# Kernel optimization log

Measured on AMD Instinct MI355X. Metric: run time of the kernel, lower is better.

Reference implementation:

```python
import jax, jax.numpy as jnp
import numpy as np

NUM_HEADS = 8
SIZES = [(80, 80), (40, 40), (20, 20), (10, 10), (5, 5)]


def _ln(x, g, b):
    m = x.mean(-1, keepdims=True)
    var = ((x - m) ** 2).mean(-1, keepdims=True)
    return (x - m) / jnp.sqrt(var + 1e-5) * g + b


def setup_inputs() -> dict:
    key = jax.random.key(0)
    ks = jax.random.split(key, 24)
    bs, c, S = 2, 256, 1024  # v_dim = embed_dim = c
    d = {}
    for i, (h, w) in enumerate(SIZES):
        d[f"q{i}"] = jax.random.normal(ks[i], (bs, c, h, w), jnp.float32)
    d["cache"] = jax.random.normal(ks[5], (bs, S, c), jnp.float32)
    d["mask"] = jax.random.randint(ks[6], (bs, S), 0, 2).astype(jnp.int32)
    d["ln_v_g"] = jnp.ones((c,), jnp.float32)
    d["ln_v_b"] = jnp.zeros((c,), jnp.float32)
    d["ln_c_g"] = jnp.ones((c,), jnp.float32)
    d["ln_c_b"] = jnp.zeros((c,), jnp.float32)
    sd = c ** -0.5
    d["Wv"] = jax.random.normal(ks[7], (c, c), jnp.float32) * sd
    d["bv"] = jnp.zeros((c,), jnp.float32)
    d["Wc"] = jax.random.normal(ks[8], (c, c), jnp.float32) * sd
    d["bc"] = jnp.zeros((c,), jnp.float32)
    d["Wvc"] = jax.random.normal(ks[9], (c, c), jnp.float32) * sd
    d["bvc"] = jnp.zeros((c,), jnp.float32)
    d["Wo"] = jax.random.normal(ks[10], (c, c), jnp.float32) * sd
    d["bo"] = jnp.zeros((c,), jnp.float32)
    d["Wg1"] = jax.random.normal(ks[11], (c, c // 2), jnp.float32) * sd
    d["bg1"] = jnp.zeros((c // 2,), jnp.float32)
    d["Wg2"] = jax.random.normal(ks[12], (c // 2, c), jnp.float32) * 0.01
    d["bg2"] = jnp.zeros((c,), jnp.float32)
    return d


def _forward(q0, q1, q2, q3, q4, cache, mask, ln_v_g, ln_v_b, ln_c_g, ln_c_b,
             Wv, bv, Wc, bc, Wvc, bvc, Wo, bo, Wg1, bg1, Wg2, bg2):
    feats = [q0, q1, q2, q3, q4]
    bs = q0.shape[0]
    sizes = [(f.shape[2], f.shape[3]) for f in feats]
    # permute_and_flatten: (bs, c, h, w) -> (bs, h*w, c), concat over levels
    v = jnp.concatenate(
        [f.reshape(bs, f.shape[1], -1).transpose(0, 2, 1) for f in feats], axis=1)
    T = v.shape[1]
    E = Wv.shape[1]
    hd = E // NUM_HEADS
    scale = hd ** -0.5

    vn = _ln(v, ln_v_g, ln_v_b)
    cn = _ln(cache, ln_c_g, ln_c_b)

    q = ((vn @ Wv + bv) * scale).reshape(bs, T, NUM_HEADS, hd).transpose(0, 2, 1, 3)
    k = (cn @ Wc + bc).reshape(bs, -1, NUM_HEADS, hd).transpose(0, 2, 1, 3)
    val = (cn @ Wvc + bvc).reshape(bs, -1, NUM_HEADS, hd).transpose(0, 2, 1, 3)

    attn = jnp.einsum('bhtd,bhsd->bhts', q, k)
    attn = jnp.clip(attn, -50000.0, 50000.0)
    mf = mask.astype(attn.dtype)  # (bs, S); zeros -> -9e15, ones kept as +1.0 (faithful)
    attn = attn + jnp.where(mf == 0, jnp.asarray(-9e15, attn.dtype), mf)[:, None, None, :]
    p = jax.nn.softmax(attn, axis=-1)  # dropout inactive in eval mode

    o = jnp.einsum('bhts,bhsd->bhtd', p, val).transpose(0, 2, 1, 3).reshape(bs, T, E)
    delta = o @ Wo + bo

    gate = jnp.tanh(jax.nn.relu(v @ Wg1 + bg1) @ Wg2 + bg2)
    new_v = (v + gate * delta).transpose(0, 2, 1)  # (bs, c, T)

    outs = []
    start = 0
    for h, w in sizes:
        outs.append(new_v[:, :, start:start + h * w].reshape(bs, -1, h, w))
        start += h * w
    return tuple(outs)


def reference(q0, q1, q2, q3, q4, cache, mask, ln_v_g, ln_v_b, ln_c_g, ln_c_b,
              Wv, bv, Wc, bc, Wvc, bvc, Wo, bo, Wg1, bg1, Wg2, bg2):
    return _forward(q0, q1, q2, q3, q4, cache, mask, ln_v_g, ln_v_b, ln_c_g, ln_c_b,
                    Wv, bv, Wc, bc, Wvc, bvc, Wo, bo, Wg1, bg1, Wg2, bg2)
```

## Files before the change

### kernel.cpp

```cpp
#include <hip/hip_runtime.h>
#include <hip/hip_bf16.h>
#include <math.h>


typedef __attribute__((ext_vector_type(8))) short short8;
typedef __attribute__((ext_vector_type(4))) float f32x4;
typedef __hip_bfloat16 bf16;

#define T_TOK 8525
#define S_TOK 1024
#define CDIM  256
#define NHEAD 8
#define BSZ   2

static __device__ __forceinline__ f32x4 mfma16(short8 a, short8 b, f32x4 c) {
  return __builtin_amdgcn_mfma_f32_16x16x32_bf16(a, b, c, 0, 0, 0);
}

static __device__ __forceinline__ float fexp2(float x) {
#if __has_builtin(__builtin_amdgcn_exp2f)
  return __builtin_amdgcn_exp2f(x);
#else
  return exp2f(x);
#endif
}

static __device__ __forceinline__ unsigned int pack_bf16(float a, float b) {
#if __has_builtin(__builtin_amdgcn_perm)
  return __builtin_amdgcn_perm(__float_as_uint(b), __float_as_uint(a), 0x07060302u);
#else
  return (__float_as_uint(a) >> 16) | (__float_as_uint(b) & 0xFFFF0000u);
#endif
}

__global__ __launch_bounds__(256) void stage1(
    const float* __restrict__ q0, const float* __restrict__ q1,
    const float* __restrict__ q2, const float* __restrict__ q3,
    const float* __restrict__ q4,
    const float* __restrict__ Wv, const float* __restrict__ Wc,
    const float* __restrict__ Wvc, const float* __restrict__ Wo,
    const float* __restrict__ Wg1, const float* __restrict__ Wg2,
    const float* __restrict__ bv, const float* __restrict__ bg1,
    const float* __restrict__ bc, const float* __restrict__ bvc,
    const float* __restrict__ cache, const float* __restrict__ ln_c_g,
    const float* __restrict__ ln_c_b, const float* __restrict__ ln_v_g,
    const float* __restrict__ ln_v_b,
    bf16* __restrict__ WqgT, bf16* __restrict__ WcvcT, bf16* __restrict__ WoT,
    bf16* __restrict__ Wg2T, float* __restrict__ biasCV,
    float* __restrict__ biasQG, bf16* __restrict__ cnb,
    float* __restrict__ vT, bf16* __restrict__ vb, bf16* __restrict__ vnb) {
  __shared__ float sm[4160];
  const int bid = blockIdx.x, tid = threadIdx.x;
  if (bid == 80) {
    biasCV[tid] = bc[tid];
    biasCV[tid + 256] = bvc[tid];
    biasQG[tid] = bv[tid];
    if (tid < 128) biasQG[256 + tid] = bg1[tid];
    return;
  }
  if (bid > 80 && bid < 593) {
    int lane = tid & 63;
    int row = (bid - 81) * 4 + (tid >> 6);
    const float* x = cache + (size_t)row * CDIM;
    float v0 = x[lane], v1 = x[lane + 64], v2 = x[lane + 128], v3 = x[lane + 192];
    float s = v0 + v1 + v2 + v3;
    float s2 = v0 * v0 + v1 * v1 + v2 * v2 + v3 * v3;
#pragma unroll
    for (int off = 1; off < 64; off <<= 1) {
      s += __shfl_xor(s, off);
      s2 += __shfl_xor(s2, off);
    }
    float mean = s * (1.f / 256.f);
    float var = s2 * (1.f / 256.f) - mean * mean;
    float rstd = rsqrtf(var + 1e-5f);
    bf16* y = cnb + (size_t)row * CDIM;
    y[lane] = __float2bfloat16((v0 - mean) * rstd * ln_c_g[lane] + ln_c_b[lane]);
    y[lane + 64] = __float2bfloat16((v1 - mean) * rstd * ln_c_g[lane + 64] + ln_c_b[lane + 64]);
    y[lane + 128] = __float2bfloat16((v2 - mean) * rstd * ln_c_g[lane + 128] + ln_c_b[lane + 128]);
    y[lane + 192] = __float2bfloat16((v3 - mean) * rstd * ln_c_g[lane + 192] + ln_c_b[lane + 192]);
    return;
  }
  if (bid < 80) {
    float (*tl)[65] = (float(*)[65])sm;
    const float* W; bf16* WT; int K, N, local;
    if (bid < 16)      { W = Wv;  WT = WqgT;           K = 256; N = 256; local = bid; }
    else if (bid < 32) { W = Wc;  WT = WcvcT;          K = 256; N = 256; local = bid - 16; }
    else if (bid < 48) { W = Wvc; WT = WcvcT + 65536;  K = 256; N = 256; local = bid - 32; }
    else if (bid < 64) { W = Wo;  WT = WoT;            K = 256; N = 256; local = bid - 48; }
    else if (bid < 72) { W = Wg1; WT = WqgT + 65536;   K = 256; N = 128; local = bid - 64; }
    else               { W = Wg2; WT = Wg2T;           K = 128; N = 256; local = bid - 72; }
    const int ktiles = K >> 6;
    const int K0 = (local % ktiles) * 64, N0 = (local / ktiles) * 64;
    const int kk = tid >> 4, n4 = (tid & 15) * 4;
#pragma unroll
    for (int i = 0; i < 4; ++i) {
      int k = kk + 16 * i;
      float4 w4 = *(const float4*)&W[(size_t)(K0 + k) * N + N0 + n4];
      tl[n4 + 0][k] = w4.x; tl[n4 + 1][k] = w4.y;
      tl[n4 + 2][k] = w4.z; tl[n4 + 3][k] = w4.w;
    }
    __syncthreads();
    const int nn = tid >> 4, k4 = (tid & 15) * 4;
#pragma unroll
    for (int i = 0; i < 4; ++i) {
      int n = nn + 16 * i;
      bf16 o[4] __attribute__((aligned(8)));
#pragma unroll
      for (int j = 0; j < 4; ++j) o[j] = __float2bfloat16(tl[n][k4 + j]);
      *(uint2*)&WT[(size_t)(N0 + n) * K + K0 + k4] = *(uint2*)o;
    }
    return;
  }
  constexpr int HW[5] = {6400, 1600, 400, 100, 25};
  constexpr int TST[5] = {0, 6400, 8000, 8400, 8500};
  constexpr int T16[5] = {0, 400, 500, 525, 532};
  float (*tile)[260] = (float(*)[260])sm;
  const int bb = bid - 593;
  const int tileid = bb % 534, b = bb / 534;
  int lvl = 0;
#pragma unroll
  for (int i = 1; i < 5; ++i) if (tileid >= T16[i]) lvl = i;
  const int p0 = (tileid - T16[lvl]) * 16;
  const int hw = HW[lvl];
  const float* src = ((lvl == 0) ? q0 : (lvl == 1) ? q1 : (lvl == 2) ? q2
                      : (lvl == 3) ? q3 : q4) + (size_t)b * CDIM * hw;
  const int pl = tid & 15, cb = tid >> 4;
  const int pg = p0 + pl;
#pragma unroll
  for (int i = 0; i < 16; ++i) {
    int c = cb + 16 * i;
    tile[pl][c] = (pg < hw) ? src[(size_t)c * hw + pg] : 0.f;
  }
  __syncthreads();
  if (pg < hw) {
    int tglob = TST[lvl] + pg;
#pragma unroll
    for (int i = 0; i < 16; ++i) {
      int c = cb + 16 * i;
      vT[((size_t)b * CDIM + c) * T_TOK + tglob] = tile[pl][c];
    }
  }
  const int lane = tid & 63, w = tid >> 6;
#pragma unroll
  for (int rr = 0; rr < 4; ++rr) {
    int row = w * 4 + rr;
    int p = p0 + row;
    if (p >= hw) continue;
    float x0 = tile[row][lane], x1 = tile[row][lane + 64],
          x2 = tile[row][lane + 128], x3 = tile[row][lane + 192];
    float s = x0 + x1 + x2 + x3;
    float s2 = x0 * x0 + x1 * x1 + x2 * x2 + x3 * x3;
#pragma unroll
    for (int off = 1; off < 64; off <<= 1) {
      s += __shfl_xor(s, off);
      s2 += __shfl_xor(s2, off);
    }
    float mean = s * (1.f / 256.f);
    float var = s2 * (1.f / 256.f) - mean * mean;
    float rstd = rsqrtf(var + 1e-5f);
    size_t base = ((size_t)b * T_TOK + TST[lvl] + p) * CDIM;
    float xs[4] = {x0, x1, x2, x3};
#pragma unroll
    for (int j = 0; j < 4; ++j) {
      int c = lane + 64 * j;
      float x = xs[j];
      vb[base + c] = __float2bfloat16(x);
      vnb[base + c] = __float2bfloat16((x - mean) * rstd * ln_v_g[c] + ln_v_b[c]);
    }
  }
}

__global__ __launch_bounds__(256) void gemm_qg(
    const bf16* __restrict__ vnb, const bf16* __restrict__ vb,
    const bf16* __restrict__ WqgT, const float* __restrict__ biasQG,
    bf16* __restrict__ qb, bf16* __restrict__ ghb, int M) {
  __shared__ __align__(16) bf16 Asl[128][136];
  __shared__ __align__(16) bf16 Bsl[64][136];
  const int tid = threadIdx.x;
  const int wave = tid >> 6, lane = tid & 63, quad = lane >> 4, l15 = lane & 15;
  const int m0 = blockIdx.y * 128;
  const int n0 = blockIdx.x * 64;
  const bf16* A = (n0 < 256) ? vnb : vb;
  f32x4 acc[2][4];
#pragma unroll
  for (int i = 0; i < 2; ++i)
#pragma unroll
    for (int j = 0; j < 4; ++j) acc[i][j] = (f32x4){0.f, 0.f, 0.f, 0.f};

  for (int k0 = 0; k0 < 256; k0 += 128) {
    __syncthreads();
#pragma unroll
    for (int c = 0; c < 8; ++c) {
      int chunk = c * 256 + tid;
      int row = chunk >> 4, col = (chunk & 15) * 8;
      int gr = m0 + row;
      if (gr >= M) gr = M - 1;
      *(uint4*)&Asl[row][col] = *(const uint4*)&A[(size_t)gr * 256 + k0 + col];
    }
#pragma unroll
    for (int c = 0; c < 4; ++c) {
      int chunk = c * 256 + tid;
      int row = chunk >> 4, col = (chunk & 15) * 8;
      *(uint4*)&Bsl[row][col] = *(const uint4*)&WqgT[(size_t)(n0 + row) * 256 + k0 + col];
    }
    __syncthreads();
#pragma unroll
    for (int kk = 0; kk < 128; kk += 32) {
      short8 af0 = *(const short8*)&Asl[wave * 32 + l15][kk + quad * 8];
      short8 af1 = *(const short8*)&Asl[wave * 32 + 16 + l15][kk + quad * 8];
      short8 bf0 = *(const short8*)&Bsl[l15][kk + quad * 8];
      short8 bf1 = *(const short8*)&Bsl[16 + l15][kk + quad * 8];
      short8 bf2 = *(const short8*)&Bsl[32 + l15][kk + quad * 8];
      short8 bf3 = *(const short8*)&Bsl[48 + l15][kk + quad * 8];
      acc[0][0] = mfma16(af0, bf0, acc[0][0]);
      acc[0][1] = mfma16(af0, bf1, acc[0][1]);
      acc[0][2] = mfma16(af0, bf2, acc[0][2]);
      acc[0][3] = mfma16(af0, bf3, acc[0][3]);
      acc[1][0] = mfma16(af1, bf0, acc[1][0]);
      acc[1][1] = mfma16(af1, bf1, acc[1][1]);
      acc[1][2] = mfma16(af1, bf2, acc[1][2]);
      acc[1][3] = mfma16(af1, bf3, acc[1][3]);
    }
  }
#pragma unroll
  for (int ms = 0; ms < 2; ++ms)
#pragma unroll
    for (int nt = 0; nt < 4; ++nt)
#pragma unroll
      for (int r = 0; r < 4; ++r) {
        int m = m0 + wave * 32 + ms * 16 + quad * 4 + r;
        if (m >= M) continue;
        int n = n0 + nt * 16 + l15;
        float x = acc[ms][nt][r] + biasQG[n];
        if (n < 256) {
          qb[(size_t)m * 256 + n] = __float2bfloat16(x * 0.25504765517f);
        } else {
          ghb[(size_t)m * 128 + (n - 256)] = __float2bfloat16(fmaxf(x, 0.f));
        }
      }
}

__global__ __launch_bounds__(256) void gemm_kval(
    const bf16* __restrict__ cnb, const bf16* __restrict__ WcvcT,
    const float* __restrict__ biasCV, bf16* __restrict__ kb,
    bf16* __restrict__ valTb, int M) {
  __shared__ __align__(16) bf16 Asl[128][136];
  __shared__ __align__(16) bf16 Bsl[64][136];
  const int tid = threadIdx.x;
  const int wave = tid >> 6, lane = tid & 63, quad = lane >> 4, l15 = lane & 15;
  const int m0 = blockIdx.y * 128;
  const int n0 = blockIdx.x * 64;
  f32x4 acc[2][4];
#pragma unroll
  for (int i = 0; i < 2; ++i)
#pragma unroll
    for (int j = 0; j < 4; ++j) acc[i][j] = (f32x4){0.f, 0.f, 0.f, 0.f};

  for (int k0 = 0; k0 < 256; k0 += 128) {
    __syncthreads();
#pragma unroll
    for (int c = 0; c < 8; ++c) {
      int chunk = c * 256 + tid;
      int row = chunk >> 4, col = (chunk & 15) * 8;
      *(uint4*)&Asl[row][col] = *(const uint4*)&cnb[(size_t)(m0 + row) * 256 + k0 + col];
    }
#pragma unroll
    for (int c = 0; c < 4; ++c) {
      int chunk = c * 256 + tid;
      int row = chunk >> 4, col = (chunk & 15) * 8;
      *(uint4*)&Bsl[row][col] = *(const uint4*)&WcvcT[(size_t)(n0 + row) * 256 + k0 + col];
    }
    __syncthreads();
#pragma unroll
    for (int kk = 0; kk < 128; kk += 32) {
      short8 af0 = *(const short8*)&Asl[wave * 32 + l15][kk + quad * 8];
      short8 af1 = *(const short8*)&Asl[wave * 32 + 16 + l15][kk + quad * 8];
      short8 bf0 = *(const short8*)&Bsl[l15][kk + quad * 8];
      short8 bf1 = *(const short8*)&Bsl[16 + l15][kk + quad * 8];
      short8 bf2 = *(const short8*)&Bsl[32 + l15][kk + quad * 8];
      short8 bf3 = *(const short8*)&Bsl[48 + l15][kk + quad * 8];
      acc[0][0] = mfma16(af0, bf0, acc[0][0]);
      acc[0][1] = mfma16(af0, bf1, acc[0][1]);
      acc[0][2] = mfma16(af0, bf2, acc[0][2]);
      acc[0][3] = mfma16(af0, bf3, acc[0][3]);
      acc[1][0] = mfma16(af1, bf0, acc[1][0]);
      acc[1][1] = mfma16(af1, bf1, acc[1][1]);
      acc[1][2] = mfma16(af1, bf2, acc[1][2]);
      acc[1][3] = mfma16(af1, bf3, acc[1][3]);
    }
  }
#pragma unroll
  for (int ms = 0; ms < 2; ++ms)
#pragma unroll
    for (int nt = 0; nt < 4; ++nt)
#pragma unroll
      for (int r = 0; r < 4; ++r) {
        int m = m0 + wave * 32 + ms * 16 + quad * 4 + r;
        int n = n0 + nt * 16 + l15;
        float x = acc[ms][nt][r] + biasCV[n];
        if (n < 256) {
          kb[(size_t)m * 256 + n] = __float2bfloat16(x);
        } else {
          int n2 = n - 256;
          int bb = m >> 10, s = m & 1023;
          int hh = n2 >> 5, d = n2 & 31;
          valTb[(((size_t)(bb * NHEAD + hh) * 32 + d) << 10) + s] = __float2bfloat16(x);
        }
      }
}

__global__ __launch_bounds__(256) void attn_kernel(
    const bf16* __restrict__ qb, const bf16* __restrict__ kb,
    const bf16* __restrict__ valTb, const int* __restrict__ mask,
    bf16* __restrict__ ob) {
  __shared__ __align__(16) bf16 Ksl[2][4096];
  __shared__ __align__(16) bf16 Vsl[2][4096];
  __shared__ __align__(16) float biasl[2][128];
  const int tid = threadIdx.x;
  const int wv = tid >> 6, lane = tid & 63, quad = lane >> 4, l15 = lane & 15;
  const int b = blockIdx.y >> 3, h = blockIdx.y & 7;
  const int t0w = blockIdx.x * 128 + wv * 32;
  int tA = t0w + l15;       if (tA >= T_TOK) tA = T_TOK - 1;
  int tB = t0w + 16 + l15;  if (tB >= T_TOK) tB = T_TOK - 1;
  short8 qf0 = *(const short8*)&qb[((size_t)b * T_TOK + tA) * CDIM + h * 32 + quad * 8];
  short8 qf1 = *(const short8*)&qb[((size_t)b * T_TOK + tB) * CDIM + h * 32 + quad * 8];
  f32x4 o0a = {0.f, 0.f, 0.f, 0.f}, o1a = {0.f, 0.f, 0.f, 0.f}, o2a = {0.f, 0.f, 0.f, 0.f};
  f32x4 o0b = {0.f, 0.f, 0.f, 0.f}, o1b = {0.f, 0.f, 0.f, 0.f}, o2b = {0.f, 0.f, 0.f, 0.f};
  const short8 ones = (short8){0x3F80, 0x3F80, 0x3F80, 0x3F80,
                               0x3F80, 0x3F80, 0x3F80, 0x3F80};
  const size_t kbase = ((size_t)b * S_TOK) * CDIM + h * 32;
  const size_t vbase = (size_t)(b * NHEAD + h) << 15;
  const int P0tab[4] = {0, 16, 4, 20};
  int kdst[2], vo1[2], vo2[2];
  size_t kofs[2], vofs[2];
#pragma unroll
  for (int c = 0; c < 2; ++c) {
    int chunk = c * 256 + tid;
    int ks = chunk >> 2, kd16 = chunk & 3;
    kdst[c] = (ks >> 4) * 512 + (ks & 15) * 32 + kd16 * 8;
    kofs[c] = (size_t)ks * CDIM + kd16 * 8;
    int vd = chunk >> 4, vs8 = (chunk & 15) * 8;
    int p1 = (vs8 >> 5) * 32 + P0tab[(vs8 >> 3) & 3];
    int p2 = p1 + 8;
    int vx = vd & 7;
    vo1[c] = vd * 128 + (((p1 >> 3) ^ vx) << 3) + (p1 & 7);
    vo2[c] = vd * 128 + (((p2 >> 3) ^ vx) << 3) + (p2 & 7);
    vofs[c] = ((size_t)vd << 10) + vs8;
  }
  const int rx = l15 & 7;

  uint4 kreg[2], vreg[2];
  float breg = 0.f;
#pragma unroll
  for (int c = 0; c < 2; ++c) {
    kreg[c] = *(const uint4*)&kb[kbase + kofs[c]];
    vreg[c] = *(const uint4*)&valTb[vbase + vofs[c]];
  }
  if (tid < 128) breg = mask[b * S_TOK + tid] ? -12.984255368f : -1e18f;
#pragma unroll
  for (int c = 0; c < 2; ++c) {
    *(uint4*)&Ksl[0][kdst[c]] = kreg[c];
    uint2 lo; lo.x = vreg[c].x; lo.y = vreg[c].y;
    uint2 hi; hi.x = vreg[c].z; hi.y = vreg[c].w;
    *(uint2*)&Vsl[0][vo1[c]] = lo;
    *(uint2*)&Vsl[0][vo2[c]] = hi;
  }
  if (tid < 128) biasl[0][tid] = breg;
  __syncthreads();

  for (int sbi = 0; sbi < 8; ++sbi) {
    const int cur = sbi & 1;
    if (sbi < 7) {
      int sb = (sbi + 1) * 128;
#pragma unroll
      for (int c = 0; c < 2; ++c) {
        kreg[c] = *(const uint4*)&kb[kbase + (size_t)sb * CDIM + kofs[c]];
        vreg[c] = *(const uint4*)&valTb[vbase + sb + vofs[c]];
      }
      if (tid < 128) breg = mask[b * S_TOK + sb + tid] ? -12.984255368f : -1e18f;
    }
#pragma unroll
    for (int ss = 0; ss < 128; ss += 32) {
      short8 kf0 = *(const short8*)&Ksl[cur][(ss >> 4) * 512 + l15 * 32 + quad * 8];
      short8 kf1 = *(const short8*)&Ksl[cur][(ss >> 4) * 512 + 512 + l15 * 32 + quad * 8];
      f32x4 bias0 = *(const f32x4*)&biasl[cur][ss + quad * 4];
      f32x4 bias1 = *(const f32x4*)&biasl[cur][ss + 16 + quad * 4];
      int vc = (ss >> 3) + quad;
      short8 vf0 = *(const short8*)&Vsl[cur][l15 * 128 + ((vc ^ rx) << 3)];
      short8 vf1 = *(const short8*)&Vsl[cur][(16 + l15) * 128 + ((vc ^ rx) << 3)];
      {
        f32x4 s0 = mfma16(kf0, qf0, bias0);
        f32x4 s1 = mfma16(kf1, qf0, bias1);
        float pa = fexp2(s0[0]), pb = fexp2(s0[1]);
        float pc = fexp2(s0[2]), pd = fexp2(s0[3]);
        float pe = fexp2(s1[0]), pf_ = fexp2(s1[1]);
        float pg = fexp2(s1[2]), ph = fexp2(s1[3]);
        uint4 pu;
        pu.x = pack_bf16(pa, pb); pu.y = pack_bf16(pc, pd);
        pu.z = pack_bf16(pe, pf_); pu.w = pack_bf16(pg, ph);
        short8 pfr = *(short8*)&pu;
        o2a = mfma16(pfr, ones, o2a);
        o0a = mfma16(pfr, vf0, o0a);
        o1a = mfma16(pfr, vf1, o1a);
      }
      {
        f32x4 s0 = mfma16(kf0, qf1, bias0);
        f32x4 s1 = mfma16(kf1, qf1, bias1);
        float pa = fexp2(s0[0]), pb = fexp2(s0[1]);
        float pc = fexp2(s0[2]), pd = fexp2(s0[3]);
        float pe = fexp2(s1[0]), pf_ = fexp2(s1[1]);
        float pg = fexp2(s1[2]), ph = fexp2(s1[3]);
        uint4 pu;
        pu.x = pack_bf16(pa, pb); pu.y = pack_bf16(pc, pd);
        pu.z = pack_bf16(pe, pf_); pu.w = pack_bf16(pg, ph);
        short8 pfr = *(short8*)&pu;
        o2b = mfma16(pfr, ones, o2b);
        o0b = mfma16(pfr, vf0, o0b);
        o1b = mfma16(pfr, vf1, o1b);
      }
    }
    if (sbi < 7) {
      const int nxt = cur ^ 1;
#pragma unroll
      for (int c = 0; c < 2; ++c) {
        *(uint4*)&Ksl[nxt][kdst[c]] = kreg[c];
        uint2 lo; lo.x = vreg[c].x; lo.y = vreg[c].y;
        uint2 hi; hi.x = vreg[c].z; hi.y = vreg[c].w;
        *(uint2*)&Vsl[nxt][vo1[c]] = lo;
        *(uint2*)&Vsl[nxt][vo2[c]] = hi;
      }
      if (tid < 128) biasl[nxt][tid] = breg;
    }
    __syncthreads();
  }
#pragma unroll
  for (int g = 0; g < 2; ++g) {
    f32x4 o0 = g ? o0b : o0a;
    f32x4 o1 = g ? o1b : o1a;
    f32x4 o2 = g ? o2b : o2a;
#pragma unroll
    for (int r = 0; r < 4; ++r) {
      int t = t0w + g * 16 + quad * 4 + r;
      if (t < T_TOK) {
        float rli = 1.0f / o2[r];
        size_t basep = ((size_t)b * T_TOK + t) * CDIM + h * 32;
        ob[basep + l15] = __float2bfloat16(o0[r] * rli);
        ob[basep + 16 + l15] = __float2bfloat16(o1[r] * rli);
      }
    }
  }
}

__global__ __launch_bounds__(256) void gemm_out(
    const bf16* __restrict__ obuf, const bf16* __restrict__ WoT,
    const float* __restrict__ bo, const bf16* __restrict__ ghb,
    const bf16* __restrict__ Wg2T, const float* __restrict__ bg2,
    const float* __restrict__ vT, float* __restrict__ out, int M) {
  constexpr int HW[5] = {6400, 1600, 400, 100, 25};
  constexpr int TST[5] = {0, 6400, 8000, 8400, 8500};
  constexpr size_t OUTOFF[5] = {0, 3276800, 4096000, 4300800, 4352000};
  __shared__ __align__(16) char smem[52224];
  bf16 (*Asl)[136] = (bf16(*)[136])smem;
  bf16 (*Bsl)[136] = (bf16(*)[136])(smem + 34816);
  float (*tile)[132] = (float(*)[132])smem;
  const int tid = threadIdx.x;
  const int wave = tid >> 6, lane = tid & 63, quad = lane >> 4, l15 = lane & 15;
  const int m0 = blockIdx.y * 128, n0 = blockIdx.x * 64;
  f32x4 aD[2][4], aG[2][4];
#pragma unroll
  for (int i = 0; i < 2; ++i)
#pragma unroll
    for (int j = 0; j < 4; ++j) {
      aD[i][j] = (f32x4){0.f, 0.f, 0.f, 0.f};
      aG[i][j] = (f32x4){0.f, 0.f, 0.f, 0.f};
    }
  for (int k0 = 0; k0 < 256; k0 += 128) {
    __syncthreads();
#pragma unroll
    for (int c = 0; c < 8; ++c) {
      int chunk = c * 256 + tid;
      int row = chunk >> 4, col = (chunk & 15) * 8;
      int gr = m0 + row;
      if (gr >= M) gr = M - 1;
      *(uint4*)&Asl[row][col] = *(const uint4*)&obuf[(size_t)gr * 256 + k0 + col];
    }
#pragma unroll
    for (int c = 0; c < 4; ++c) {
      int chunk = c * 256 + tid;
      int row = chunk >> 4, col = (chunk & 15) * 8;
      *(uint4*)&Bsl[row][col] = *(const uint4*)&WoT[(size_t)(n0 + row) * 256 + k0 + col];
    }
    __syncthreads();
#pragma unroll
    for (int kk = 0; kk < 128; kk += 32) {
      short8 af0 = *(const short8*)&Asl[wave * 32 + l15][kk + quad * 8];
      short8 af1 = *(const short8*)&Asl[wave * 32 + 16 + l15][kk + quad * 8];
#pragma unroll
      for (int j = 0; j < 4; ++j) {
        short8 bfj = *(const short8*)&Bsl[j * 16 + l15][kk + quad * 8];
        aD[0][j] = mfma16(af0, bfj, aD[0][j]);
        aD[1][j] = mfma16(af1, bfj, aD[1][j]);
      }
    }
  }
  __syncthreads();
#pragma unroll
  for (int c = 0; c < 8; ++c) {
    int chunk = c * 256 + tid;
    int row = chunk >> 4, col = (chunk & 15) * 8;
    int gr = m0 + row;
    if (gr >= M) gr = M - 1;
    *(uint4*)&Asl[row][col] = *(const uint4*)&ghb[(size_t)gr * 128 + col];
  }
#pragma unroll
  for (int c = 0; c < 4; ++c) {
    int chunk = c * 256 + tid;
    int row = chunk >> 4, col = (chunk & 15) * 8;
    *(uint4*)&Bsl[row][col] = *(const uint4*)&Wg2T[(size_t)(n0 + row) * 128 + col];
  }
  __syncthreads();
#pragma unroll
  for (int kk = 0; kk < 128; kk += 32) {
    short8 af0 = *(const short8*)&Asl[wave * 32 + l15][kk + quad * 8];
    short8 af1 = *(const short8*)&Asl[wave * 32 + 16 + l15][kk + quad * 8];
#pragma unroll
    for (int j = 0; j < 4; ++j) {
      short8 bfj = *(const short8*)&Bsl[j * 16 + l15][kk + quad * 8];
      aG[0][j] = mfma16(af0, bfj, aG[0][j]);
      aG[1][j] = mfma16(af1, bfj, aG[1][j]);
    }
  }
  __syncthreads();
#pragma unroll
  for (int ms = 0; ms < 2; ++ms)
#pragma unroll
    for (int nt = 0; nt < 4; ++nt) {
      int n = n0 + nt * 16 + l15;
      float bod = bo[n], bgd = bg2[n];
      float4 res;
      float tmp[4];
#pragma unroll
      for (int r = 0; r < 4; ++r) {
        float xd = aD[ms][nt][r] + bod;
        float xg = aG[ms][nt][r] + bgd;
        float xc = fminf(fmaxf(xg, -15.f), 15.f);
        float e = __expf(2.f * xc);
        float gt = (e - 1.f) / (e + 1.f);
        tmp[r] = gt * xd;
      }
      res.x = tmp[0]; res.y = tmp[1]; res.z = tmp[2]; res.w = tmp[3];
      *(float4*)&tile[nt * 16 + l15][wave * 32 + ms * 16 + quad * 4] = res;
    }
  __syncthreads();
  const int tl = tid & 127, c2 = tid >> 7;
  const int t = m0 + tl;
  const bool valid = t < M;
  int bb = (t >= T_TOK) ? 1 : 0;
  int tt = t - bb * T_TOK;
  if (tt >= T_TOK) tt = T_TOK - 1;
  int lvl = 0;
#pragma unroll
  for (int i = 1; i < 5; ++i) if (tt >= TST[i]) lvl = i;
  const int p = tt - TST[lvl], hw = HW[lvl];
  float* dst = out + OUTOFF[lvl] + ((size_t)bb * CDIM + n0) * hw + p;
  const float* vsrc = vT + ((size_t)bb * CDIM + n0) * T_TOK + tt;
#pragma unroll
  for (int c0 = 0; c0 < 32; ++c0) {
    int c = c0 * 2 + c2;
    if (valid) dst[(size_t)c * hw] = vsrc[(size_t)c * T_TOK] + tile[c][tl];
  }
}

extern "C" void kernel_launch(void* const* d_in, const int* in_sizes, int n_in,
                              void* d_out, int out_size, void* d_ws, size_t ws_size,
                              hipStream_t stream) {
  const float* q0 = (const float*)d_in[0];
  const float* q1 = (const float*)d_in[1];
  const float* q2 = (const float*)d_in[2];
  const float* q3 = (const float*)d_in[3];
  const float* q4 = (const float*)d_in[4];
  const float* cache = (const float*)d_in[5];
  const int* mask = (const int*)d_in[6];
  const float* ln_v_g = (const float*)d_in[7];
  const float* ln_v_b = (const float*)d_in[8];
  const float* ln_c_g = (const float*)d_in[9];
  const float* ln_c_b = (const float*)d_in[10];
  const float* Wv = (const float*)d_in[11];
  const float* bv = (const float*)d_in[12];
  const float* Wc = (const float*)d_in[13];
  const float* bc = (const float*)d_in[14];
  const float* Wvc = (const float*)d_in[15];
  const float* bvc = (const float*)d_in[16];
  const float* Wo = (const float*)d_in[17];
  const float* bo = (const float*)d_in[18];
  const float* Wg1 = (const float*)d_in[19];
  const float* bg1 = (const float*)d_in[20];
  const float* Wg2 = (const float*)d_in[21];
  const float* bg2 = (const float*)d_in[22];
  float* out = (float*)d_out;

  const int R = BSZ * T_TOK;
  const size_t RC = (size_t)R * CDIM;
  const size_t SC = (size_t)BSZ * S_TOK * CDIM;

  char* p = (char*)d_ws;
  float* vT = (float*)p;           p += RC * 4;
  bf16* vb = (bf16*)p;             p += RC * 2;
  bf16* vnb = (bf16*)p;            p += RC * 2;
  bf16* qb = (bf16*)p;             p += RC * 2;
  bf16* ob = (bf16*)p;             p += RC * 2;
  bf16* ghb = (bf16*)p;            p += (size_t)R * 128 * 2;
  bf16* cnb = (bf16*)p;            p += SC * 2;
  bf16* kb = (bf16*)p;             p += SC * 2;
  bf16* valTb = (bf16*)p;          p += SC * 2;
  bf16* WqgT = (bf16*)p;           p += 98304 * 2;
  bf16* WcvcT = (bf16*)p;          p += 131072 * 2;
  bf16* WoT = (bf16*)p;            p += 65536 * 2;
  bf16* Wg2T = (bf16*)p;           p += 32768 * 2;
  float* biasCV = (float*)p;       p += 512 * 4;
  float* biasQG = (float*)p;       p += 384 * 4;

  stage1<<<dim3(1661), dim3(256), 0, stream>>>(
      q0, q1, q2, q3, q4, Wv, Wc, Wvc, Wo, Wg1, Wg2, bv, bg1, bc, bvc,
      cache, ln_c_g, ln_c_b, ln_v_g, ln_v_b,
      WqgT, WcvcT, WoT, Wg2T, biasCV, biasQG, cnb, vT, vb, vnb);
  gemm_qg<<<dim3(6, 134), dim3(256), 0, stream>>>(
      vnb, vb, WqgT, biasQG, qb, ghb, R);
  gemm_kval<<<dim3(8, 16), dim3(256), 0, stream>>>(
      cnb, WcvcT, biasCV, kb, valTb, BSZ * S_TOK);
  attn_kernel<<<dim3(67, BSZ * NHEAD), dim3(256), 0, stream>>>(
      qb, kb, valTb, mask, ob);
  gemm_out<<<dim3(4, 134), dim3(256), 0, stream>>>(
      ob, WoT, bo, ghb, Wg2T, bg2, vT, out, R);
}
```

Measured before the change: 210.7 us.

## Single-buffer attention LDS tiles and store V in K-like fragment layout

The attention kernel drops double-buffered LDS for K, V and mask bias in favour of single buffers, adding an extra barrier before each refill. V is written to LDS in the same blocked fragment layout as K, so both fragments are read with one shared index instead of an XOR swizzle. This halves LDS use, which may raise occupancy and simplify addressing, but the extra barrier per block stalls all waves until compute on the current tile finishes.

```diff
diff --git a/kernel.cpp b/kernel.cpp
--- a/kernel.cpp
+++ b/kernel.cpp
@@ -313,11 +313,11 @@
     const bf16* __restrict__ qb, const bf16* __restrict__ kb,
     const bf16* __restrict__ valTb, const int* __restrict__ mask,
     bf16* __restrict__ ob) {
-  __shared__ __align__(16) bf16 Ksl[2][4096];
-  __shared__ __align__(16) bf16 Vsl[2][4096];
-  __shared__ __align__(16) float biasl[2][128];
+  __shared__ __align__(16) bf16 Ksl[4096];
+  __shared__ __align__(16) bf16 Vsl[4096];
+  __shared__ __align__(16) float biasl[128];
   const int tid = threadIdx.x;
-  const int wv = tid >> 6, lane = tid & 63, quad = lane >> 4, l15 = lane & 15;
+  const int lane = tid & 63, wv = tid >> 6, quad = lane >> 4, l15 = lane & 15;
   const int b = blockIdx.y >> 3, h = blockIdx.y & 7;
   const int t0w = blockIdx.x * 128 + wv * 32;
   int tA = t0w + l15;       if (tA >= T_TOK) tA = T_TOK - 1;
@@ -330,8 +330,7 @@
                                0x3F80, 0x3F80, 0x3F80, 0x3F80};
   const size_t kbase = ((size_t)b * S_TOK) * CDIM + h * 32;
   const size_t vbase = (size_t)(b * NHEAD + h) << 15;
-  const int P0tab[4] = {0, 16, 4, 20};
-  int kdst[2], vo1[2], vo2[2];
+  int kdst[2], vd1[2], vd2[2];
   size_t kofs[2], vofs[2];
 #pragma unroll
   for (int c = 0; c < 2; ++c) {
@@ -340,14 +339,15 @@
     kdst[c] = (ks >> 4) * 512 + (ks & 15) * 32 + kd16 * 8;
     kofs[c] = (size_t)ks * CDIM + kd16 * 8;
     int vd = chunk >> 4, vs8 = (chunk & 15) * 8;
-    int p1 = (vs8 >> 5) * 32 + P0tab[(vs8 >> 3) & 3];
-    int p2 = p1 + 8;
-    int vx = vd & 7;
-    vo1[c] = vd * 128 + (((p1 >> 3) ^ vx) << 3) + (p1 & 7);
-    vo2[c] = vd * 128 + (((p2 >> 3) ^ vx) << 3) + (p2 & 7);
+    int schunk = vs8 >> 5, sb = vs8 & 31;
+    int kb1 = (((sb >> 2) & 3) << 3) + (((sb >> 4) & 1) << 2);
+    int sb2 = sb + 4;
+    int kb2 = (((sb2 >> 2) & 3) << 3) + (((sb2 >> 4) & 1) << 2);
+    int base = schunk * 1024 + (vd >> 4) * 512 + (vd & 15) * 32;
+    vd1[c] = base + kb1;
+    vd2[c] = base + kb2;
     vofs[c] = ((size_t)vd << 10) + vs8;
   }
-  const int rx = l15 & 7;
 
   uint4 kreg[2], vreg[2];
   float breg = 0.f;
@@ -359,17 +359,16 @@
   if (tid < 128) breg = mask[b * S_TOK + tid] ? -12.984255368f : -1e18f;
 #pragma unroll
   for (int c = 0; c < 2; ++c) {
-    *(uint4*)&Ksl[0][kdst[c]] = kreg[c];
+    *(uint4*)&Ksl[kdst[c]] = kreg[c];
     uint2 lo; lo.x = vreg[c].x; lo.y = vreg[c].y;
     uint2 hi; hi.x = vreg[c].z; hi.y = vreg[c].w;
-    *(uint2*)&Vsl[0][vo1[c]] = lo;
-    *(uint2*)&Vsl[0][vo2[c]] = hi;
-  }
-  if (tid < 128) biasl[0][tid] = breg;
+    *(uint2*)&Vsl[vd1[c]] = lo;
+    *(uint2*)&Vsl[vd2[c]] = hi;
+  }
+  if (tid < 128) biasl[tid] = breg;
   __syncthreads();
 
   for (int sbi = 0; sbi < 8; ++sbi) {
-    const int cur = sbi & 1;
     if (sbi < 7) {
       int sb = (sbi + 1) * 128;
 #pragma unroll
@@ -381,13 +380,13 @@
     }
 #pragma unroll
     for (int ss = 0; ss < 128; ss += 32) {
-      short8 kf0 = *(const short8*)&Ksl[cur][(ss >> 4) * 512 + l15 * 32 + quad * 8];
-      short8 kf1 = *(const short8*)&Ksl[cur][(ss >> 4) * 512 + 512 + l15 * 32 + quad * 8];
-      f32x4 bias0 = *(const f32x4*)&biasl[cur][ss + quad * 4];
-      f32x4 bias1 = *(const f32x4*)&biasl[cur][ss + 16 + quad * 4];
-      int vc = (ss >> 3) + quad;
-      short8 vf0 = *(const short8*)&Vsl[cur][l15 * 128 + ((vc ^ rx) << 3)];
-      short8 vf1 = *(const short8*)&Vsl[cur][(16 + l15) * 128 + ((vc ^ rx) << 3)];
+      const int cb = (ss >> 5) * 1024 + l15 * 32 + quad * 8;
+      short8 kf0 = *(const short8*)&Ksl[cb];
+      short8 kf1 = *(const short8*)&Ksl[cb + 512];
+      short8 vf0 = *(const short8*)&Vsl[cb];
+      short8 vf1 = *(const short8*)&Vsl[cb + 512];
+      f32x4 bias0 = *(const f32x4*)&biasl[ss + quad * 4];
+      f32x4 bias1 = *(const f32x4*)&biasl[ss + 16 + quad * 4];
       {
         f32x4 s0 = mfma16(kf0, qf0, bias0);
         f32x4 s1 = mfma16(kf1, qf0, bias1);
@@ -420,18 +419,18 @@
       }
     }
     if (sbi < 7) {
-      const int nxt = cur ^ 1;
+      __syncthreads();
 #pragma unroll
       for (int c = 0; c < 2; ++c) {
-        *(uint4*)&Ksl[nxt][kdst[c]] = kreg[c];
+        *(uint4*)&Ksl[kdst[c]] = kreg[c];
         uint2 lo; lo.x = vreg[c].x; lo.y = vreg[c].y;
         uint2 hi; hi.x = vreg[c].z; hi.y = vreg[c].w;
-        *(uint2*)&Vsl[nxt][vo1[c]] = lo;
-        *(uint2*)&Vsl[nxt][vo2[c]] = hi;
-      }
-      if (tid < 128) biasl[nxt][tid] = breg;
-    }
-    __syncthreads();
+        *(uint2*)&Vsl[vd1[c]] = lo;
+        *(uint2*)&Vsl[vd2[c]] = hi;
+      }
+      if (tid < 128) biasl[tid] = breg;
+      __syncthreads();
+    }
   }
 #pragma unroll
   for (int g = 0; g < 2; ++g) {
```

New measurement: 220.8 us. 4.8% more time.

## Use 8 waves per attention block with 16 tokens each and coalesced output store

Applied to the files above, without the earlier changes.

The attention kernel now launches 512 threads per block, and each wave handles 16 query tokens instead of 32, which doubles the wave count for the same tile. Each thread loads one K/V chunk instead of two, and V is stored in shared memory in the same blocked layout as K, so the XOR swizzle is gone. Output is staged through shared memory so each lane writes a 16-byte vector to global memory instead of scattered bf16 stores. The aim is better latency hiding and coalesced writes. In exchange, each wave reuses its K/V shared-memory fragments across fewer tokens, so LDS reads per MFMA double, and the unswizzled V layout may cause bank conflicts.

```diff
diff --git a/kernel.cpp b/kernel.cpp
--- a/kernel.cpp
+++ b/kernel.cpp
@@ -309,7 +309,7 @@
       }
 }
 
-__global__ __launch_bounds__(256) void attn_kernel(
+__global__ __launch_bounds__(512) void attn_kernel(
     const bf16* __restrict__ qb, const bf16* __restrict__ kb,
     const bf16* __restrict__ valTb, const int* __restrict__ mask,
     bf16* __restrict__ ob) {
@@ -317,53 +317,41 @@
   __shared__ __align__(16) bf16 Vsl[2][4096];
   __shared__ __align__(16) float biasl[2][128];
   const int tid = threadIdx.x;
-  const int wv = tid >> 6, lane = tid & 63, quad = lane >> 4, l15 = lane & 15;
+  const int lane = tid & 63, wv = tid >> 6, quad = lane >> 4, l15 = lane & 15;
   const int b = blockIdx.y >> 3, h = blockIdx.y & 7;
-  const int t0w = blockIdx.x * 128 + wv * 32;
-  int tA = t0w + l15;       if (tA >= T_TOK) tA = T_TOK - 1;
-  int tB = t0w + 16 + l15;  if (tB >= T_TOK) tB = T_TOK - 1;
-  short8 qf0 = *(const short8*)&qb[((size_t)b * T_TOK + tA) * CDIM + h * 32 + quad * 8];
-  short8 qf1 = *(const short8*)&qb[((size_t)b * T_TOK + tB) * CDIM + h * 32 + quad * 8];
-  f32x4 o0a = {0.f, 0.f, 0.f, 0.f}, o1a = {0.f, 0.f, 0.f, 0.f}, o2a = {0.f, 0.f, 0.f, 0.f};
-  f32x4 o0b = {0.f, 0.f, 0.f, 0.f}, o1b = {0.f, 0.f, 0.f, 0.f}, o2b = {0.f, 0.f, 0.f, 0.f};
+  const int t0w = blockIdx.x * 128 + wv * 16;
+  int tA = t0w + l15;
+  if (tA >= T_TOK) tA = T_TOK - 1;
+  short8 qf = *(const short8*)&qb[((size_t)b * T_TOK + tA) * CDIM + h * 32 + quad * 8];
+  f32x4 o0 = {0.f, 0.f, 0.f, 0.f};
+  f32x4 o1 = {0.f, 0.f, 0.f, 0.f};
+  f32x4 o2 = {0.f, 0.f, 0.f, 0.f};
   const short8 ones = (short8){0x3F80, 0x3F80, 0x3F80, 0x3F80,
                                0x3F80, 0x3F80, 0x3F80, 0x3F80};
   const size_t kbase = ((size_t)b * S_TOK) * CDIM + h * 32;
   const size_t vbase = (size_t)(b * NHEAD + h) << 15;
-  const int P0tab[4] = {0, 16, 4, 20};
-  int kdst[2], vo1[2], vo2[2];
-  size_t kofs[2], vofs[2];
-#pragma unroll
-  for (int c = 0; c < 2; ++c) {
-    int chunk = c * 256 + tid;
-    int ks = chunk >> 2, kd16 = chunk & 3;
-    kdst[c] = (ks >> 4) * 512 + (ks & 15) * 32 + kd16 * 8;
-    kofs[c] = (size_t)ks * CDIM + kd16 * 8;
-    int vd = chunk >> 4, vs8 = (chunk & 15) * 8;
-    int p1 = (vs8 >> 5) * 32 + P0tab[(vs8 >> 3) & 3];
-    int p2 = p1 + 8;
-    int vx = vd & 7;
-    vo1[c] = vd * 128 + (((p1 >> 3) ^ vx) << 3) + (p1 & 7);
-    vo2[c] = vd * 128 + (((p2 >> 3) ^ vx) << 3) + (p2 & 7);
-    vofs[c] = ((size_t)vd << 10) + vs8;
-  }
-  const int rx = l15 & 7;
-
-  uint4 kreg[2], vreg[2];
+  const int ks = tid >> 2, kd16 = tid & 3;
+  const int kdst = (ks >> 4) * 512 + (ks & 15) * 32 + kd16 * 8;
+  const size_t kofs = (size_t)ks * CDIM + kd16 * 8;
+  const int vd = tid >> 4, vs8 = (tid & 15) * 8;
+  const int schunk = vs8 >> 5, sb_ = vs8 & 31;
+  const int kb1 = (((sb_ >> 2) & 3) << 3) + (((sb_ >> 4) & 1) << 2);
+  const int sb2_ = sb_ + 4;
+  const int kb2 = (((sb2_ >> 2) & 3) << 3) + (((sb2_ >> 4) & 1) << 2);
+  const int vbl = schunk * 1024 + (vd >> 4) * 512 + (vd & 15) * 32;
+  const int vd1 = vbl + kb1, vd2 = vbl + kb2;
+  const size_t vofs = ((size_t)vd << 10) + vs8;
+
+  uint4 kreg = *(const uint4*)&kb[kbase + kofs];
+  uint4 vreg = *(const uint4*)&valTb[vbase + vofs];
   float breg = 0.f;
-#pragma unroll
-  for (int c = 0; c < 2; ++c) {
-    kreg[c] = *(const uint4*)&kb[kbase + kofs[c]];
-    vreg[c] = *(const uint4*)&valTb[vbase + vofs[c]];
-  }
   if (tid < 128) breg = mask[b * S_TOK + tid] ? -12.984255368f : -1e18f;
-#pragma unroll
-  for (int c = 0; c < 2; ++c) {
-    *(uint4*)&Ksl[0][kdst[c]] = kreg[c];
-    uint2 lo; lo.x = vreg[c].x; lo.y = vreg[c].y;
-    uint2 hi; hi.x = vreg[c].z; hi.y = vreg[c].w;
-    *(uint2*)&Vsl[0][vo1[c]] = lo;
-    *(uint2*)&Vsl[0][vo2[c]] = hi;
+  *(uint4*)&Ksl[0][kdst] = kreg;
+  {
+    uint2 lo; lo.x = vreg.x; lo.y = vreg.y;
+    uint2 hi; hi.x = vreg.z; hi.y = vreg.w;
+    *(uint2*)&Vsl[0][vd1] = lo;
+    *(uint2*)&Vsl[0][vd2] = hi;
   }
   if (tid < 128) biasl[0][tid] = breg;
   __syncthreads();
@@ -372,82 +360,59 @@
     const int cur = sbi & 1;
     if (sbi < 7) {
       int sb = (sbi + 1) * 128;
-#pragma unroll
-      for (int c = 0; c < 2; ++c) {
-        kreg[c] = *(const uint4*)&kb[kbase + (size_t)sb * CDIM + kofs[c]];
-        vreg[c] = *(const uint4*)&valTb[vbase + sb + vofs[c]];
-      }
+      kreg = *(const uint4*)&kb[kbase + (size_t)sb * CDIM + kofs];
+      vreg = *(const uint4*)&valTb[vbase + sb + vofs];
       if (tid < 128) breg = mask[b * S_TOK + sb + tid] ? -12.984255368f : -1e18f;
     }
 #pragma unroll
     for (int ss = 0; ss < 128; ss += 32) {
-      short8 kf0 = *(const short8*)&Ksl[cur][(ss >> 4) * 512 + l15 * 32 + quad * 8];
-      short8 kf1 = *(const short8*)&Ksl[cur][(ss >> 4) * 512 + 512 + l15 * 32 + quad * 8];
+      const int cb = (ss >> 5) * 1024 + l15 * 32 + quad * 8;
+      short8 kf0 = *(const short8*)&Ksl[cur][cb];
+      short8 kf1 = *(const short8*)&Ksl[cur][cb + 512];
+      short8 vf0 = *(const short8*)&Vsl[cur][cb];
+      short8 vf1 = *(const short8*)&Vsl[cur][cb + 512];
       f32x4 bias0 = *(const f32x4*)&biasl[cur][ss + quad * 4];
       f32x4 bias1 = *(const f32x4*)&biasl[cur][ss + 16 + quad * 4];
-      int vc = (ss >> 3) + quad;
-      short8 vf0 = *(const short8*)&Vsl[cur][l15 * 128 + ((vc ^ rx) << 3)];
-      short8 vf1 = *(const short8*)&Vsl[cur][(16 + l15) * 128 + ((vc ^ rx) << 3)];
-      {
-        f32x4 s0 = mfma16(kf0, qf0, bias0);
-        f32x4 s1 = mfma16(kf1, qf0, bias1);
-        float pa = fexp2(s0[0]), pb = fexp2(s0[1]);
-        float pc = fexp2(s0[2]), pd = fexp2(s0[3]);
-        float pe = fexp2(s1[0]), pf_ = fexp2(s1[1]);
-        float pg = fexp2(s1[2]), ph = fexp2(s1[3]);
-        uint4 pu;
-        pu.x = pack_bf16(pa, pb); pu.y = pack_bf16(pc, pd);
-        pu.z = pack_bf16(pe, pf_); pu.w = pack_bf16(pg, ph);
-        short8 pfr = *(short8*)&pu;
-        o2a = mfma16(pfr, ones, o2a);
-        o0a = mfma16(pfr, vf0, o0a);
-        o1a = mfma16(pfr, vf1, o1a);
-      }
-      {
-        f32x4 s0 = mfma16(kf0, qf1, bias0);
-        f32x4 s1 = mfma16(kf1, qf1, bias1);
-        float pa = fexp2(s0[0]), pb = fexp2(s0[1]);
-        float pc = fexp2(s0[2]), pd = fexp2(s0[3]);
-        float pe = fexp2(s1[0]), pf_ = fexp2(s1[1]);
-        float pg = fexp2(s1[2]), ph = fexp2(s1[3]);
-        uint4 pu;
-        pu.x = pack_bf16(pa, pb); pu.y = pack_bf16(pc, pd);
-        pu.z = pack_bf16(pe, pf_); pu.w = pack_bf16(pg, ph);
-        short8 pfr = *(short8*)&pu;
-        o2b = mfma16(pfr, ones, o2b);
-        o0b = mfma16(pfr, vf0, o0b);
-        o1b = mfma16(pfr, vf1, o1b);
-      }
+      f32x4 s0 = mfma16(kf0, qf, bias0);
+      f32x4 s1 = mfma16(kf1, qf, bias1);
+      float pa = fexp2(s0[0]), pb = fexp2(s0[1]);
+      float pc = fexp2(s0[2]), pd = fexp2(s0[3]);
+      float pe = fexp2(s1[0]), pf_ = fexp2(s1[1]);
+      float pg = fexp2(s1[2]), ph = fexp2(s1[3]);
+      uint4 pu;
+      pu.x = pack_bf16(pa, pb); pu.y = pack_bf16(pc, pd);
+      pu.z = pack_bf16(pe, pf_); pu.w = pack_bf16(pg, ph);
+      short8 pfr = *(short8*)&pu;
+      o2 = mfma16(pfr, ones, o2);
+      o0 = mfma16(pfr, vf0, o0);
+      o1 = mfma16(pfr, vf1, o1);
     }
     if (sbi < 7) {
       const int nxt = cur ^ 1;
-#pragma unroll
-      for (int c = 0; c < 2; ++c) {
-        *(uint4*)&Ksl[nxt][kdst[c]] = kreg[c];
-        uint2 lo; lo.x = vreg[c].x; lo.y = vreg[c].y;
-        uint2 hi; hi.x = vreg[c].z; hi.y = vreg[c].w;
-        *(uint2*)&Vsl[nxt][vo1[c]] = lo;
-        *(uint2*)&Vsl[nxt][vo2[c]] = hi;
-      }
+      *(uint4*)&Ksl[nxt][kdst] = kreg;
+      uint2 lo; lo.x = vreg.x; lo.y = vreg.y;
+      uint2 hi; hi.x = vreg.z; hi.y = vreg.w;
+      *(uint2*)&Vsl[nxt][vd1] = lo;
+      *(uint2*)&Vsl[nxt][vd2] = hi;
       if (tid < 128) biasl[nxt][tid] = breg;
     }
     __syncthreads();
   }
-#pragma unroll
-  for (int g = 0; g < 2; ++g) {
-    f32x4 o0 = g ? o0b : o0a;
-    f32x4 o1 = g ? o1b : o1a;
-    f32x4 o2 = g ? o2b : o2a;
-#pragma unroll
-    for (int r = 0; r < 4; ++r) {
-      int t = t0w + g * 16 + quad * 4 + r;
-      if (t < T_TOK) {
-        float rli = 1.0f / o2[r];
-        size_t basep = ((size_t)b * T_TOK + t) * CDIM + h * 32;
-        ob[basep + l15] = __float2bfloat16(o0[r] * rli);
-        ob[basep + 16 + l15] = __float2bfloat16(o1[r] * rli);
-      }
-    }
+  bf16* tile = &Ksl[0][0] + wv * 512;
+#pragma unroll
+  for (int r = 0; r < 4; ++r) {
+    float rli = 1.0f / o2[r];
+    int tl = quad * 4 + r;
+    tile[tl * 32 + l15] = __float2bfloat16(o0[r] * rli);
+    tile[tl * 32 + 16 + l15] = __float2bfloat16(o1[r] * rli);
+  }
+  {
+    int tl = lane >> 2;
+    int d8 = (lane & 3) * 8;
+    int t = t0w + tl;
+    uint4 val = *(const uint4*)&tile[tl * 32 + d8];
+    if (t < T_TOK)
+      *(uint4*)&ob[((size_t)b * T_TOK + t) * CDIM + h * 32 + d8] = val;
   }
 }
 
@@ -628,7 +593,7 @@
       vnb, vb, WqgT, biasQG, qb, ghb, R);
   gemm_kval<<<dim3(8, 16), dim3(256), 0, stream>>>(
       cnb, WcvcT, biasCV, kb, valTb, BSZ * S_TOK);
-  attn_kernel<<<dim3(67, BSZ * NHEAD), dim3(256), 0, stream>>>(
+  attn_kernel<<<dim3(67, BSZ * NHEAD), dim3(512), 0, stream>>>(
       qb, kb, valTb, mask, ob);
   gemm_out<<<dim3(4, 134), dim3(256), 0, stream>>>(
       ob, WoT, bo, ghb, Wg2T, bg2, vT, out, R);
```

Result: no change. 213.0 us (+1.1%).
